# Kernel optimization log

Hardware: AMD Instinct MI355X
Metric: run time of the kernel (lower is better)

## Reference

```python
import jax, jax.numpy as jnp
import numpy as np

B, T, F = 8192, 30, 16
H1, H2 = 64, 32


def _lstm(x, Wih, Whh, b):
    """PyTorch-convention LSTM (gate order i,f,g,o). x: [B,T,I] -> (ys [B,T,H], hT [B,H])."""
    H = Whh.shape[1]
    h0 = jnp.zeros((x.shape[0], H), x.dtype)

    def step(carry, xt):
        h, c = carry
        z = xt @ Wih.T + h @ Whh.T + b  # [B,4H]
        i, f, g, o = jnp.split(z, 4, axis=-1)
        c = jax.nn.sigmoid(f) * c + jax.nn.sigmoid(i) * jnp.tanh(g)
        h = jax.nn.sigmoid(o) * jnp.tanh(c)
        return (h, c), h

    (hT, _), ys = jax.lax.scan(step, (h0, h0), jnp.swapaxes(x, 0, 1))
    return jnp.swapaxes(ys, 0, 1), hT


def setup_inputs() -> dict:
    key = jax.random.key(0)
    ks = jax.random.split(key, 16)
    s = 0.1  # small init scale for numerical sanity
    return {
        "x": jax.random.normal(ks[0], (B, T, F), jnp.float32),
        "Wih1": jax.random.normal(ks[1], (4 * H1, F), jnp.float32) * s,
        "Whh1": jax.random.normal(ks[2], (4 * H1, H1), jnp.float32) * s,
        "b1": jax.random.normal(ks[3], (4 * H1,), jnp.float32) * s,
        "Wih2": jax.random.normal(ks[4], (4 * H2, H1), jnp.float32) * s,
        "Whh2": jax.random.normal(ks[5], (4 * H2, H2), jnp.float32) * s,
        "b2": jax.random.normal(ks[6], (4 * H2,), jnp.float32) * s,
        "Wih3": jax.random.normal(ks[7], (4 * H2, H2), jnp.float32) * s,
        "Whh3": jax.random.normal(ks[8], (4 * H2, H2), jnp.float32) * s,
        "b3": jax.random.normal(ks[9], (4 * H2,), jnp.float32) * s,
        "Wih4": jax.random.normal(ks[10], (4 * H1, H2), jnp.float32) * s,
        "Whh4": jax.random.normal(ks[11], (4 * H1, H1), jnp.float32) * s,
        "b4": jax.random.normal(ks[12], (4 * H1,), jnp.float32) * s,
        "Wout": jax.random.normal(ks[13], (F, H1), jnp.float32) * s,
        "bout": jax.random.normal(ks[14], (F,), jnp.float32) * s,
    }


def reference(x, Wih1, Whh1, b1, Wih2, Whh2, b2, Wih3, Whh3, b3, Wih4, Whh4, b4, Wout, bout):
    ys1, _ = _lstm(x, Wih1, Whh1, b1)          # encoder LSTM(64)
    _, latent = _lstm(ys1, Wih2, Whh2, b2)      # encoder LSTM(32) -> final hidden [B,32]
    repeated = jnp.broadcast_to(latent[:, None, :], (latent.shape[0], T, latent.shape[1]))
    ys3, _ = _lstm(repeated, Wih3, Whh3, b3)    # decoder LSTM(32)
    ys4, _ = _lstm(ys3, Wih4, Whh4, b4)         # decoder LSTM(64)
    return ys4 @ Wout.T + bout                  # [B,T,F]
```

## Files before the change

### kernel.cpp

```cpp
#include <hip/hip_runtime.h>


#define TT 30
#define FF 16

typedef unsigned short u16t;
typedef __attribute__((ext_vector_type(8))) short short8;
typedef __attribute__((ext_vector_type(4))) short short4v;
typedef __attribute__((ext_vector_type(4))) float floatx4;

#define MFMA(a, b, c) __builtin_amdgcn_mfma_f32_16x16x32_bf16(a, b, c, 0, 0, 0)

__device__ __forceinline__ float rcpf(float v) { return __builtin_amdgcn_rcpf(v); }
__device__ __forceinline__ float sigf(float v) { return rcpf(1.f + __expf(-v)); }
__device__ __forceinline__ float tanhf_(float v) { return 1.f - 2.f * rcpf(1.f + __expf(2.f * v)); }
__device__ __forceinline__ u16t f2bf(float f) {
  unsigned int u = __float_as_uint(f);
  u = (u + 0x7FFFu + ((u >> 16) & 1u)) >> 16;
  return (u16t)u;
}
__device__ __forceinline__ short8 ldFrag(const float* p) {
  const float4 lo = *(const float4*)p;
  const float4 hi = *(const float4*)(p + 4);
  short8 r;
  r[0] = (short)f2bf(lo.x); r[1] = (short)f2bf(lo.y);
  r[2] = (short)f2bf(lo.z); r[3] = (short)f2bf(lo.w);
  r[4] = (short)f2bf(hi.x); r[5] = (short)f2bf(hi.y);
  r[6] = (short)f2bf(hi.z); r[7] = (short)f2bf(hi.w);
  return r;
}
__device__ __forceinline__ float cellUp(const floatx4 acc, float& c) {
  float iv = sigf(acc[0]), fv = sigf(acc[1]);
  float gv = tanhf_(acc[2]), ov = sigf(acc[3]);
  c = fv * c + iv * gv;
  return ov * tanhf_(c);
}

__global__ __launch_bounds__(512, 4) void lstm_ae_mfma3(
    const float* __restrict__ x,
    const float* __restrict__ Wih1, const float* __restrict__ Whh1, const float* __restrict__ b1,
    const float* __restrict__ Wih2, const float* __restrict__ Whh2, const float* __restrict__ b2,
    const float* __restrict__ Wih3, const float* __restrict__ Whh3, const float* __restrict__ b3,
    const float* __restrict__ Wih4, const float* __restrict__ Whh4, const float* __restrict__ b4,
    const float* __restrict__ Wout, const float* __restrict__ bout,
    float* __restrict__ out)
{
  __shared__ __align__(16) u16t xAll[16 * 968];
  __shared__ __align__(16) u16t aB[16 * 264];

  const int t = threadIdx.x;
  const int w = t >> 6, lane = t & 63;
  const int q = lane >> 4, n = lane & 15;
  const int q8 = q * 8, n264 = n * 264, n968 = n * 968;
  const int bBase = blockIdx.x * 16;
  const int nlo = n >> 2, ngt = n & 3;
  const u16t* aRow = &aB[n264];

  for (int i = t; i < 16 * 264; i += 512) aB[i] = 0;
  {
    const float* xb = x + (size_t)bBase * (TT * FF);
    for (int i4 = t; i4 < 1920; i4 += 512) {
      int e = i4 * 4;
      int b = e / 480, r = e - b * 480;
      int stp = r >> 4, f = r & 15;
      float4 v = *(const float4*)&xb[e];
      short4v s4 = { (short)f2bf(v.x), (short)f2bf(v.y), (short)f2bf(v.z), (short)f2bf(v.w) };
      *(short4v*)&xAll[b * 968 + stp * 32 + f] = s4;
    }
    for (int i = t; i < 7680; i += 512) {
      int b = i / 480, r = i - b * 480;
      int stp = r >> 4, f = r & 15;
      xAll[b * 968 + stp * 32 + 16 + f] = 0;
    }
  }
  short8 w1f[2][3]; floatx4 bias1[2];
  const short8 z8 = { 0, 0, 0, 0, 0, 0, 0, 0 };
#pragma unroll
  for (int tt = 0; tt < 2; ++tt) {
    int row = ngt * 64 + (2 * w + tt) * 4 + nlo;
    w1f[tt][0] = z8;
    if (q < 2) w1f[tt][0] = ldFrag(&Wih1[row * 16 + q8]);
    w1f[tt][1] = ldFrag(&Whh1[row * 64 + q8]);
    w1f[tt][2] = ldFrag(&Whh1[row * 64 + 32 + q8]);
#pragma unroll
    for (int r = 0; r < 4; ++r) bias1[tt][r] = b1[r * 64 + (2 * w + tt) * 4 + q];
  }
  short8 w2f[3]; floatx4 bias2;
  {
    int row = ngt * 32 + w * 4 + nlo;
    w2f[0] = ldFrag(&Wih2[row * 64 + q8]);
    w2f[1] = ldFrag(&Wih2[row * 64 + 32 + q8]);
    w2f[2] = ldFrag(&Whh2[row * 32 + q8]);
#pragma unroll
    for (int r = 0; r < 4; ++r) bias2[r] = b2[r * 32 + w * 4 + q];
  }
  __syncthreads();

  float c1v[2] = {0.f, 0.f}, c2v = 0.f;

  {
    const short8 bx = *(const short8*)&xAll[n968 + q8];
    floatx4 a0 = bias1[0], a1 = bias1[1];
    a0 = MFMA(w1f[0][0], bx, a0); a1 = MFMA(w1f[1][0], bx, a1);
    aB[n264 + (2 * w) * 4 + q]     = f2bf(cellUp(a0, c1v[0]));
    aB[n264 + (2 * w + 1) * 4 + q] = f2bf(cellUp(a1, c1v[1]));
  }
  __syncthreads();

  for (int st = 0; st < TT - 1; ++st) {
    const int p = st & 1;
    const short8 bh1a = *(const short8*)&aRow[p * 64 + q8];
    const short8 bh1b = *(const short8*)&aRow[p * 64 + 32 + q8];
    const short8 bh2  = *(const short8*)&aRow[128 + (1 - p) * 32 + q8];
    const short8 bx   = *(const short8*)&xAll[n968 + (st + 1) * 32 + q8];
    floatx4 a2 = bias2;
    a2 = MFMA(w2f[0], bh1a, a2);
    a2 = MFMA(w2f[1], bh1b, a2);
    a2 = MFMA(w2f[2], bh2, a2);
    floatx4 a0 = bias1[0], a1 = bias1[1];
    a0 = MFMA(w1f[0][0], bx, a0);   a1 = MFMA(w1f[1][0], bx, a1);
    a0 = MFMA(w1f[0][1], bh1a, a0); a1 = MFMA(w1f[1][1], bh1a, a1);
    a0 = MFMA(w1f[0][2], bh1b, a0); a1 = MFMA(w1f[1][2], bh1b, a1);
    aB[n264 + 128 + p * 32 + w * 4 + q]        = f2bf(cellUp(a2, c2v));
    aB[n264 + (1 - p) * 64 + (2 * w) * 4 + q]  = f2bf(cellUp(a0, c1v[0]));
    aB[n264 + (1 - p) * 64 + (2 * w + 1) * 4 + q] = f2bf(cellUp(a1, c1v[1]));
    __syncthreads();
  }
  {
    const short8 bh1a = *(const short8*)&aRow[64 + q8];
    const short8 bh1b = *(const short8*)&aRow[96 + q8];
    const short8 bh2  = *(const short8*)&aRow[128 + q8];
    floatx4 a2 = bias2;
    a2 = MFMA(w2f[0], bh1a, a2);
    a2 = MFMA(w2f[1], bh1b, a2);
    a2 = MFMA(w2f[2], bh2, a2);
    aB[n264 + 160 + w * 4 + q] = f2bf(cellUp(a2, c2v));
  }
  __syncthreads();

  short8 w3f[2]; floatx4 bias3;
  {
    int row = ngt * 32 + w * 4 + nlo;
    w3f[0] = ldFrag(&Wih3[row * 32 + q8]);
    w3f[1] = ldFrag(&Whh3[row * 32 + q8]);
#pragma unroll
    for (int r = 0; r < 4; ++r) bias3[r] = b3[r * 32 + w * 4 + q];
  }
  short8 w4f[2][3]; floatx4 bias4[2];
#pragma unroll
  for (int tt = 0; tt < 2; ++tt) {
    int row = ngt * 64 + (2 * w + tt) * 4 + nlo;
    w4f[tt][0] = ldFrag(&Wih4[row * 32 + q8]);
    w4f[tt][1] = ldFrag(&Whh4[row * 64 + q8]);
    w4f[tt][2] = ldFrag(&Whh4[row * 64 + 32 + q8]);
#pragma unroll
    for (int r = 0; r < 4; ++r) bias4[tt][r] = b4[r * 64 + (2 * w + tt) * 4 + q];
  }
  short8 wof[2];
  wof[0] = ldFrag(&Wout[n * 64 + q8]);
  wof[1] = ldFrag(&Wout[n * 64 + 32 + q8]);
  const floatx4 biasO = *(const floatx4*)&bout[q * 4];
  const short8 blat = *(const short8*)&aRow[160 + q8];
  for (int i = t; i < 1024; i += 512) aB[(i >> 6) * 264 + 64 + (i & 63)] = 0;
  __syncthreads();

  float c3v = 0.f, c4v[2] = {0.f, 0.f};

  {
    floatx4 a3 = bias3;
    a3 = MFMA(w3f[0], blat, a3);
    aB[n264 + 192 + w * 4 + q] = f2bf(cellUp(a3, c3v));
  }
  __syncthreads();

  for (int st = 0; st < TT - 1; ++st) {
    const int p = st & 1;
    const short8 bh3  = *(const short8*)&aRow[192 + p * 32 + q8];
    const short8 bh4a = *(const short8*)&aRow[(1 - p) * 64 + q8];
    const short8 bh4b = *(const short8*)&aRow[(1 - p) * 64 + 32 + q8];
    floatx4 a40 = bias4[0], a41 = bias4[1];
    a40 = MFMA(w4f[0][0], bh3, a40);  a41 = MFMA(w4f[1][0], bh3, a41);
    a40 = MFMA(w4f[0][1], bh4a, a40); a41 = MFMA(w4f[1][1], bh4a, a41);
    a40 = MFMA(w4f[0][2], bh4b, a40); a41 = MFMA(w4f[1][2], bh4b, a41);
    floatx4 a3 = bias3;
    a3 = MFMA(w3f[0], blat, a3);
    a3 = MFMA(w3f[1], bh3, a3);
    aB[n264 + p * 64 + (2 * w) * 4 + q]     = f2bf(cellUp(a40, c4v[0]));
    aB[n264 + p * 64 + (2 * w + 1) * 4 + q] = f2bf(cellUp(a41, c4v[1]));
    aB[n264 + 192 + (1 - p) * 32 + w * 4 + q] = f2bf(cellUp(a3, c3v));
    if (st > 0 && w == ((st - 1) & 7)) {
      floatx4 yv = biasO;
      yv = MFMA(wof[0], bh4a, yv);
      yv = MFMA(wof[1], bh4b, yv);
      *(floatx4*)&out[((size_t)(bBase + n) * TT + (st - 1)) * FF + q * 4] = yv;
    }
    __syncthreads();
  }
  {
    const short8 bh3  = *(const short8*)&aRow[224 + q8];
    const short8 bh4a = *(const short8*)&aRow[q8];
    const short8 bh4b = *(const short8*)&aRow[32 + q8];
    floatx4 a40 = bias4[0], a41 = bias4[1];
    a40 = MFMA(w4f[0][0], bh3, a40);  a41 = MFMA(w4f[1][0], bh3, a41);
    a40 = MFMA(w4f[0][1], bh4a, a40); a41 = MFMA(w4f[1][1], bh4a, a41);
    a40 = MFMA(w4f[0][2], bh4b, a40); a41 = MFMA(w4f[1][2], bh4b, a41);
    aB[n264 + 64 + (2 * w) * 4 + q]     = f2bf(cellUp(a40, c4v[0]));
    aB[n264 + 64 + (2 * w + 1) * 4 + q] = f2bf(cellUp(a41, c4v[1]));
    if (w == 4) {
      floatx4 yv = biasO;
      yv = MFMA(wof[0], bh4a, yv);
      yv = MFMA(wof[1], bh4b, yv);
      *(floatx4*)&out[((size_t)(bBase + n) * TT + 28) * FF + q * 4] = yv;
    }
  }
  __syncthreads();
  if (w == 5) {
    const short8 ba = *(const short8*)&aRow[64 + q8];
    const short8 bb = *(const short8*)&aRow[96 + q8];
    floatx4 yv = biasO;
    yv = MFMA(wof[0], ba, yv);
    yv = MFMA(wof[1], bb, yv);
    *(floatx4*)&out[((size_t)(bBase + n) * TT + 29) * FF + q * 4] = yv;
  }
}

extern "C" void kernel_launch(void* const* d_in, const int* in_sizes, int n_in,
                              void* d_out, int out_size, void* d_ws, size_t ws_size,
                              hipStream_t stream) {
  const float* x    = (const float*)d_in[0];
  const float* Wih1 = (const float*)d_in[1];
  const float* Whh1 = (const float*)d_in[2];
  const float* b1   = (const float*)d_in[3];
  const float* Wih2 = (const float*)d_in[4];
  const float* Whh2 = (const float*)d_in[5];
  const float* b2   = (const float*)d_in[6];
  const float* Wih3 = (const float*)d_in[7];
  const float* Whh3 = (const float*)d_in[8];
  const float* b3   = (const float*)d_in[9];
  const float* Wih4 = (const float*)d_in[10];
  const float* Whh4 = (const float*)d_in[11];
  const float* b4   = (const float*)d_in[12];
  const float* Wout = (const float*)d_in[13];
  const float* bout = (const float*)d_in[14];
  float* out = (float*)d_out;

  const int B = in_sizes[0] / (TT * FF);
  dim3 grid(B / 16), block(512);
  lstm_ae_mfma3<<<grid, block, 0, stream>>>(
      x, Wih1, Whh1, b1, Wih2, Whh2, b2, Wih3, Whh3, b3,
      Wih4, Whh4, b4, Wout, bout, out);
}
```

Before: 171.7 us.

## Split LSTM gate tiles across 16 waves and stage biases in LDS

Measured after the change: 175.8 us. +2.4%, slower.

```diff
diff --git a/kernel.cpp b/kernel.cpp
--- a/kernel.cpp
+++ b/kernel.cpp
@@ -10,6 +10,8 @@
 typedef __attribute__((ext_vector_type(4))) float floatx4;
 
 #define MFMA(a, b, c) __builtin_amdgcn_mfma_f32_16x16x32_bf16(a, b, c, 0, 0, 0)
+
+template <int P> struct IC { static constexpr int v = P; };
 
 __device__ __forceinline__ float rcpf(float v) { return __builtin_amdgcn_rcpf(v); }
 __device__ __forceinline__ float sigf(float v) { return rcpf(1.f + __expf(-v)); }
@@ -36,7 +38,7 @@
   return ov * tanhf_(c);
 }
 
-__global__ __launch_bounds__(512, 4) void lstm_ae_mfma3(
+__global__ __launch_bounds__(1024, 8) void lstm_ae_mfma4(
     const float* __restrict__ x,
     const float* __restrict__ Wih1, const float* __restrict__ Whh1, const float* __restrict__ b1,
     const float* __restrict__ Wih2, const float* __restrict__ Whh2, const float* __restrict__ b2,
@@ -47,6 +49,7 @@
 {
   __shared__ __align__(16) u16t xAll[16 * 968];
   __shared__ __align__(16) u16t aB[16 * 264];
+  __shared__ __align__(16) float bSS[784];
 
   const int t = threadIdx.x;
   const int w = t >> 6, lane = t & 63;
@@ -55,11 +58,13 @@
   const int bBase = blockIdx.x * 16;
   const int nlo = n >> 2, ngt = n & 3;
   const u16t* aRow = &aB[n264];
-
-  for (int i = t; i < 16 * 264; i += 512) aB[i] = 0;
+  const bool heavy = (w >= 8);
+  const int wh = w & 7;
+
+  for (int i = t; i < 16 * 264; i += 1024) aB[i] = 0;
   {
     const float* xb = x + (size_t)bBase * (TT * FF);
-    for (int i4 = t; i4 < 1920; i4 += 512) {
+    for (int i4 = t; i4 < 1920; i4 += 1024) {
       int e = i4 * 4;
       int b = e / 480, r = e - b * 480;
       int stp = r >> 4, f = r & 15;
@@ -67,147 +72,151 @@
       short4v s4 = { (short)f2bf(v.x), (short)f2bf(v.y), (short)f2bf(v.z), (short)f2bf(v.w) };
       *(short4v*)&xAll[b * 968 + stp * 32 + f] = s4;
     }
-    for (int i = t; i < 7680; i += 512) {
+    for (int i = t; i < 7680; i += 1024) {
       int b = i / 480, r = i - b * 480;
       int stp = r >> 4, f = r & 15;
       xAll[b * 968 + stp * 32 + 16 + f] = 0;
     }
   }
-  short8 w1f[2][3]; floatx4 bias1[2];
+  for (int i = t; i < 784; i += 1024) {
+    float v;
+    if (i < 256)      { int T = i >> 4, rm = i & 15;      v = b1[(rm & 3) * 64 + T * 4 + (rm >> 2)]; }
+    else if (i < 384) { int j = i - 256, T = j >> 4, rm = j & 15; v = b2[(rm & 3) * 32 + T * 4 + (rm >> 2)]; }
+    else if (i < 512) { int j = i - 384, T = j >> 4, rm = j & 15; v = b3[(rm & 3) * 32 + T * 4 + (rm >> 2)]; }
+    else if (i < 768) { int j = i - 512, T = j >> 4, rm = j & 15; v = b4[(rm & 3) * 64 + T * 4 + (rm >> 2)]; }
+    else              { v = bout[i - 768]; }
+    bSS[i] = v;
+  }
   const short8 z8 = { 0, 0, 0, 0, 0, 0, 0, 0 };
-#pragma unroll
-  for (int tt = 0; tt < 2; ++tt) {
-    int row = ngt * 64 + (2 * w + tt) * 4 + nlo;
-    w1f[tt][0] = z8;
-    if (q < 2) w1f[tt][0] = ldFrag(&Wih1[row * 16 + q8]);
-    w1f[tt][1] = ldFrag(&Whh1[row * 64 + q8]);
-    w1f[tt][2] = ldFrag(&Whh1[row * 64 + 32 + q8]);
-#pragma unroll
-    for (int r = 0; r < 4; ++r) bias1[tt][r] = b1[r * 64 + (2 * w + tt) * 4 + q];
-  }
-  short8 w2f[3]; floatx4 bias2;
-  {
-    int row = ngt * 32 + w * 4 + nlo;
+  short8 w1f[3];
+  {
+    int row = ngt * 64 + w * 4 + nlo;
+    w1f[0] = z8;
+    if (q < 2) w1f[0] = ldFrag(&Wih1[row * 16 + q8]);
+    w1f[1] = ldFrag(&Whh1[row * 64 + q8]);
+    w1f[2] = ldFrag(&Whh1[row * 64 + 32 + q8]);
+  }
+  short8 w2f[3];
+  if (heavy) {
+    int row = ngt * 32 + wh * 4 + nlo;
     w2f[0] = ldFrag(&Wih2[row * 64 + q8]);
     w2f[1] = ldFrag(&Wih2[row * 64 + 32 + q8]);
     w2f[2] = ldFrag(&Whh2[row * 32 + q8]);
-#pragma unroll
-    for (int r = 0; r < 4; ++r) bias2[r] = b2[r * 32 + w * 4 + q];
-  }
-  __syncthreads();
-
-  float c1v[2] = {0.f, 0.f}, c2v = 0.f;
+  } else { w2f[0] = z8; w2f[1] = z8; w2f[2] = z8; }
+  __syncthreads();
+
+  float c1v = 0.f, c2v = 0.f;
 
   {
     const short8 bx = *(const short8*)&xAll[n968 + q8];
-    floatx4 a0 = bias1[0], a1 = bias1[1];
-    a0 = MFMA(w1f[0][0], bx, a0); a1 = MFMA(w1f[1][0], bx, a1);
-    aB[n264 + (2 * w) * 4 + q]     = f2bf(cellUp(a0, c1v[0]));
-    aB[n264 + (2 * w + 1) * 4 + q] = f2bf(cellUp(a1, c1v[1]));
-  }
-  __syncthreads();
-
-  for (int st = 0; st < TT - 1; ++st) {
-    const int p = st & 1;
+    floatx4 a0 = *(const floatx4*)&bSS[w * 16 + q * 4];
+    a0 = MFMA(w1f[0], bx, a0);
+    aB[n264 + w * 4 + q] = f2bf(cellUp(a0, c1v));
+  }
+  __syncthreads();
+
+  auto stepA = [&](int st, auto pc) {
+    constexpr int p = decltype(pc)::v;
     const short8 bh1a = *(const short8*)&aRow[p * 64 + q8];
     const short8 bh1b = *(const short8*)&aRow[p * 64 + 32 + q8];
-    const short8 bh2  = *(const short8*)&aRow[128 + (1 - p) * 32 + q8];
     const short8 bx   = *(const short8*)&xAll[n968 + (st + 1) * 32 + q8];
-    floatx4 a2 = bias2;
+    floatx4 a0 = *(const floatx4*)&bSS[w * 16 + q * 4];
+    a0 = MFMA(w1f[0], bx, a0);
+    a0 = MFMA(w1f[1], bh1a, a0);
+    a0 = MFMA(w1f[2], bh1b, a0);
+    if (heavy) {
+      const short8 bh2 = *(const short8*)&aRow[128 + (1 - p) * 32 + q8];
+      floatx4 a2 = *(const floatx4*)&bSS[256 + wh * 16 + q * 4];
+      a2 = MFMA(w2f[0], bh1a, a2);
+      a2 = MFMA(w2f[1], bh1b, a2);
+      a2 = MFMA(w2f[2], bh2, a2);
+      aB[n264 + 128 + p * 32 + wh * 4 + q] = f2bf(cellUp(a2, c2v));
+    }
+    aB[n264 + (1 - p) * 64 + w * 4 + q] = f2bf(cellUp(a0, c1v));
+    __syncthreads();
+  };
+  for (int st = 0; st < 28; st += 2) { stepA(st, IC<0>{}); stepA(st + 1, IC<1>{}); }
+  stepA(28, IC<0>{});
+  if (heavy) {
+    const short8 bh1a = *(const short8*)&aRow[64 + q8];
+    const short8 bh1b = *(const short8*)&aRow[96 + q8];
+    const short8 bh2  = *(const short8*)&aRow[128 + q8];
+    floatx4 a2 = *(const floatx4*)&bSS[256 + wh * 16 + q * 4];
     a2 = MFMA(w2f[0], bh1a, a2);
     a2 = MFMA(w2f[1], bh1b, a2);
     a2 = MFMA(w2f[2], bh2, a2);
-    floatx4 a0 = bias1[0], a1 = bias1[1];
-    a0 = MFMA(w1f[0][0], bx, a0);   a1 = MFMA(w1f[1][0], bx, a1);
-    a0 = MFMA(w1f[0][1], bh1a, a0); a1 = MFMA(w1f[1][1], bh1a, a1);
-    a0 = MFMA(w1f[0][2], bh1b, a0); a1 = MFMA(w1f[1][2], bh1b, a1);
-    aB[n264 + 128 + p * 32 + w * 4 + q]        = f2bf(cellUp(a2, c2v));
-    aB[n264 + (1 - p) * 64 + (2 * w) * 4 + q]  = f2bf(cellUp(a0, c1v[0]));
-    aB[n264 + (1 - p) * 64 + (2 * w + 1) * 4 + q] = f2bf(cellUp(a1, c1v[1]));
-    __syncthreads();
-  }
-  {
-    const short8 bh1a = *(const short8*)&aRow[64 + q8];
-    const short8 bh1b = *(const short8*)&aRow[96 + q8];
-    const short8 bh2  = *(const short8*)&aRow[128 + q8];
-    floatx4 a2 = bias2;
-    a2 = MFMA(w2f[0], bh1a, a2);
-    a2 = MFMA(w2f[1], bh1b, a2);
-    a2 = MFMA(w2f[2], bh2, a2);
-    aB[n264 + 160 + w * 4 + q] = f2bf(cellUp(a2, c2v));
-  }
-  __syncthreads();
-
-  short8 w3f[2]; floatx4 bias3;
-  {
-    int row = ngt * 32 + w * 4 + nlo;
+    aB[n264 + 160 + wh * 4 + q] = f2bf(cellUp(a2, c2v));
+  }
+  __syncthreads();
+
+  short8 w4f[3];
+  {
+    int row = ngt * 64 + w * 4 + nlo;
+    w4f[0] = ldFrag(&Wih4[row * 32 + q8]);
+    w4f[1] = ldFrag(&Whh4[row * 64 + q8]);
+    w4f[2] = ldFrag(&Whh4[row * 64 + 32 + q8]);
+  }
+  short8 w3f[2];
+  if (heavy) {
+    int row = ngt * 32 + wh * 4 + nlo;
     w3f[0] = ldFrag(&Wih3[row * 32 + q8]);
     w3f[1] = ldFrag(&Whh3[row * 32 + q8]);
-#pragma unroll
-    for (int r = 0; r < 4; ++r) bias3[r] = b3[r * 32 + w * 4 + q];
-  }
-  short8 w4f[2][3]; floatx4 bias4[2];
-#pragma unroll
-  for (int tt = 0; tt < 2; ++tt) {
-    int row = ngt * 64 + (2 * w + tt) * 4 + nlo;
-    w4f[tt][0] = ldFrag(&Wih4[row * 32 + q8]);
-    w4f[tt][1] = ldFrag(&Whh4[row * 64 + q8]);
-    w4f[tt][2] = ldFrag(&Whh4[row * 64 + 32 + q8]);
-#pragma unroll
-    for (int r = 0; r < 4; ++r) bias4[tt][r] = b4[r * 64 + (2 * w + tt) * 4 + q];
-  }
+  } else { w3f[0] = z8; w3f[1] = z8; }
   short8 wof[2];
-  wof[0] = ldFrag(&Wout[n * 64 + q8]);
-  wof[1] = ldFrag(&Wout[n * 64 + 32 + q8]);
-  const floatx4 biasO = *(const floatx4*)&bout[q * 4];
+  if (!heavy) {
+    wof[0] = ldFrag(&Wout[n * 64 + q8]);
+    wof[1] = ldFrag(&Wout[n * 64 + 32 + q8]);
+  } else { wof[0] = z8; wof[1] = z8; }
   const short8 blat = *(const short8*)&aRow[160 + q8];
-  for (int i = t; i < 1024; i += 512) aB[(i >> 6) * 264 + 64 + (i & 63)] = 0;
-  __syncthreads();
-
-  float c3v = 0.f, c4v[2] = {0.f, 0.f};
-
-  {
-    floatx4 a3 = bias3;
+  for (int i = t; i < 1024; i += 1024) aB[(i >> 6) * 264 + 64 + (i & 63)] = 0;
+  __syncthreads();
+
+  float c3v = 0.f, c4v = 0.f;
+
+  if (heavy) {
+    floatx4 a3 = *(const floatx4*)&bSS[384 + wh * 16 + q * 4];
     a3 = MFMA(w3f[0], blat, a3);
-    aB[n264 + 192 + w * 4 + q] = f2bf(cellUp(a3, c3v));
-  }
-  __syncthreads();
-
-  for (int st = 0; st < TT - 1; ++st) {
-    const int p = st & 1;
+    aB[n264 + 192 + wh * 4 + q] = f2bf(cellUp(a3, c3v));
+  }
+  __syncthreads();
+
+  auto stepB = [&](int st, auto pc) {
+    constexpr int p = decltype(pc)::v;
     const short8 bh3  = *(const short8*)&aRow[192 + p * 32 + q8];
     const short8 bh4a = *(const short8*)&aRow[(1 - p) * 64 + q8];
     const short8 bh4b = *(const short8*)&aRow[(1 - p) * 64 + 32 + q8];
-    floatx4 a40 = bias4[0], a41 = bias4[1];
-    a40 = MFMA(w4f[0][0], bh3, a40);  a41 = MFMA(w4f[1][0], bh3, a41);
-    a40 = MFMA(w4f[0][1], bh4a, a40); a41 = MFMA(w4f[1][1], bh4a, a41);
-    a40 = MFMA(w4f[0][2], bh4b, a40); a41 = MFMA(w4f[1][2], bh4b, a41);
-    floatx4 a3 = bias3;
-    a3 = MFMA(w3f[0], blat, a3);
-    a3 = MFMA(w3f[1], bh3, a3);
-    aB[n264 + p * 64 + (2 * w) * 4 + q]     = f2bf(cellUp(a40, c4v[0]));
-    aB[n264 + p * 64 + (2 * w + 1) * 4 + q] = f2bf(cellUp(a41, c4v[1]));
-    aB[n264 + 192 + (1 - p) * 32 + w * 4 + q] = f2bf(cellUp(a3, c3v));
-    if (st > 0 && w == ((st - 1) & 7)) {
-      floatx4 yv = biasO;
+    floatx4 a4 = *(const floatx4*)&bSS[512 + w * 16 + q * 4];
+    a4 = MFMA(w4f[0], bh3, a4);
+    a4 = MFMA(w4f[1], bh4a, a4);
+    a4 = MFMA(w4f[2], bh4b, a4);
+    if (heavy) {
+      floatx4 a3 = *(const floatx4*)&bSS[384 + wh * 16 + q * 4];
+      a3 = MFMA(w3f[0], blat, a3);
+      a3 = MFMA(w3f[1], bh3, a3);
+      aB[n264 + 192 + (1 - p) * 32 + wh * 4 + q] = f2bf(cellUp(a3, c3v));
+    }
+    aB[n264 + p * 64 + w * 4 + q] = f2bf(cellUp(a4, c4v));
+    if (!heavy && st > 0 && w == ((st - 1) & 7)) {
+      floatx4 yv = *(const floatx4*)&bSS[768 + q * 4];
       yv = MFMA(wof[0], bh4a, yv);
       yv = MFMA(wof[1], bh4b, yv);
       *(floatx4*)&out[((size_t)(bBase + n) * TT + (st - 1)) * FF + q * 4] = yv;
     }
     __syncthreads();
-  }
+  };
+  for (int st = 0; st < 28; st += 2) { stepB(st, IC<0>{}); stepB(st + 1, IC<1>{}); }
+  stepB(28, IC<0>{});
   {
     const short8 bh3  = *(const short8*)&aRow[224 + q8];
     const short8 bh4a = *(const short8*)&aRow[q8];
     const short8 bh4b = *(const short8*)&aRow[32 + q8];
-    floatx4 a40 = bias4[0], a41 = bias4[1];
-    a40 = MFMA(w4f[0][0], bh3, a40);  a41 = MFMA(w4f[1][0], bh3, a41);
-    a40 = MFMA(w4f[0][1], bh4a, a40); a41 = MFMA(w4f[1][1], bh4a, a41);
-    a40 = MFMA(w4f[0][2], bh4b, a40); a41 = MFMA(w4f[1][2], bh4b, a41);
-    aB[n264 + 64 + (2 * w) * 4 + q]     = f2bf(cellUp(a40, c4v[0]));
-    aB[n264 + 64 + (2 * w + 1) * 4 + q] = f2bf(cellUp(a41, c4v[1]));
+    floatx4 a4 = *(const floatx4*)&bSS[512 + w * 16 + q * 4];
+    a4 = MFMA(w4f[0], bh3, a4);
+    a4 = MFMA(w4f[1], bh4a, a4);
+    a4 = MFMA(w4f[2], bh4b, a4);
+    aB[n264 + 64 + w * 4 + q] = f2bf(cellUp(a4, c4v));
     if (w == 4) {
-      floatx4 yv = biasO;
+      floatx4 yv = *(const floatx4*)&bSS[768 + q * 4];
       yv = MFMA(wof[0], bh4a, yv);
       yv = MFMA(wof[1], bh4b, yv);
       *(floatx4*)&out[((size_t)(bBase + n) * TT + 28) * FF + q * 4] = yv;
@@ -217,7 +226,7 @@
   if (w == 5) {
     const short8 ba = *(const short8*)&aRow[64 + q8];
     const short8 bb = *(const short8*)&aRow[96 + q8];
-    floatx4 yv = biasO;
+    floatx4 yv = *(const floatx4*)&bSS[768 + q * 4];
     yv = MFMA(wof[0], ba, yv);
     yv = MFMA(wof[1], bb, yv);
     *(floatx4*)&out[((size_t)(bBase + n) * TT + 29) * FF + q * 4] = yv;
@@ -245,8 +254,8 @@
   float* out = (float*)d_out;
 
   const int B = in_sizes[0] / (TT * FF);
-  dim3 grid(B / 16), block(512);
-  lstm_ae_mfma3<<<grid, block, 0, stream>>>(
+  dim3 grid(B / 16), block(1024);
+  lstm_ae_mfma4<<<grid, block, 0, stream>>>(
       x, Wih1, Whh1, b1, Wih2, Whh2, b2, Wih3, Whh3, b3,
       Wih4, Whh4, b4, Wout, bout, out);
 }
```
